# Kernel optimization log

Hardware: AMD Instinct MI355X
Metric: run time of the kernel (lower is better)

The kernel has to match this reference:

```python
import jax, jax.numpy as jnp
import numpy as np

B, L, D, HD, DC = 2, 2048, 2048, 64, 2048
NH = D // HD  # 32 heads


def _rms_norm(x, eps):
    return x * jax.lax.rsqrt(jnp.mean(jnp.square(x), axis=-1, keepdims=True) + eps)


def _apply_rope(x, rope):
    # x: [b,h,l,d]; rope: [2,l,d]. x_hat = interleave(-x_odd, x_even)
    x2 = x.reshape(*x.shape[:-1], HD // 2, 2)
    x_hat = jnp.stack([-x2[..., 1], x2[..., 0]], axis=-1).reshape(x.shape)
    return x * rope[0] + x_hat * rope[1]


def setup_inputs() -> dict:
    key = jax.random.key(0)
    ks = jax.random.split(key, 6)
    return {
        "x": jax.random.normal(ks[0], (B, L, D), jnp.float32),
        "condition": jax.random.normal(ks[1], (B, DC), jnp.float32),
        "rope": jax.random.normal(ks[2], (2, L, HD), jnp.float32),
        "w_ada": jax.random.normal(ks[3], (2 * D, DC), jnp.float32) * 0.02,
        "w_qkv": jax.random.normal(ks[4], (3 * D, D), jnp.float32) * 0.02,
        "w_out": jax.random.normal(ks[5], (D, D), jnp.float32) * 0.02,
        "qk_w": jnp.ones((HD,), jnp.float32),
    }


def reference(x, condition, rope, w_ada, w_qkv, w_out, qk_w):
    eps = jnp.finfo(x.dtype).eps
    # AdaRMSNorm
    ss = (condition @ w_ada.T)[:, None, :]          # [b,1,2D]
    shift, scale = jnp.split(ss, 2, axis=-1)
    h = _rms_norm(x, eps) * (1.0 + scale) + shift   # [b,l,D]
    # fused QKV projection: 'b l (n h d)'
    qkv = (h @ w_qkv.T).reshape(B, L, 3, NH, HD)
    qkv = jnp.transpose(qkv, (2, 0, 3, 1, 4))       # [3,b,h,l,d]
    q, k, v = qkv[0], qkv[1], qkv[2]
    # per-head RMSNorm (with affine weight) + RoPE
    q = _apply_rope(_rms_norm(q, eps) * qk_w, rope)
    k = _apply_rope(_rms_norm(k, eps) * qk_w, rope)
    # SDPA
    scores = jnp.einsum('bhqd,bhkd->bhqk', q, k) / jnp.sqrt(jnp.asarray(HD, x.dtype))
    attn = jax.nn.softmax(scores, axis=-1)
    o = jnp.einsum('bhqk,bhkd->bhqd', attn, v)      # [b,h,l,d]
    o = jnp.transpose(o, (0, 2, 1, 3)).reshape(B, L, D)
    return o @ w_out.T
```

## Files before the change

kernel.cpp:

```cpp
#include <hip/hip_runtime.h>


typedef __bf16 bf16x8 __attribute__((ext_vector_type(8)));
typedef float  f32x4  __attribute__((ext_vector_type(4)));
typedef float  f32x16 __attribute__((ext_vector_type(16)));

#define EPS_F32 1.1920929e-07f
#define QSCALE 0.18033688011112042f

#if defined(__has_builtin)
#  if __has_builtin(__builtin_amdgcn_exp2f)
#    define EXP2F(x) __builtin_amdgcn_exp2f(x)
#  else
#    define EXP2F(x) __expf((x) * 0.6931471805599453f)
#  endif
#  if __has_builtin(__builtin_amdgcn_rcpf)
#    define RCPF(x) __builtin_amdgcn_rcpf(x)
#  else
#    define RCPF(x) (1.0f / (x))
#  endif
#else
#  define EXP2F(x) __expf((x) * 0.6931471805599453f)
#  define RCPF(x) (1.0f / (x))
#endif

__device__ __forceinline__ float bf2f(unsigned int u16) {
  union { unsigned int i; float f; } v; v.i = (u16 & 0xffffu) << 16; return v.f;
}
__device__ __forceinline__ unsigned short f2bf(float f) {
  union { float f; unsigned int i; } v; v.f = f;
  unsigned int r = v.i + 0x7fffu + ((v.i >> 16) & 1u);
  return (unsigned short)(r >> 16);
}
__device__ __forceinline__ unsigned int f2bf_rn_u(float f) {
  union { float f; unsigned int i; } v; v.f = f;
  return v.i + 0x8000u;
}

__device__ __forceinline__ void gload16(const void* g, void* l) {
  __builtin_amdgcn_global_load_lds(
      (const __attribute__((address_space(1))) unsigned int*)(unsigned long long)g,
      (__attribute__((address_space(3))) unsigned int*)(unsigned int)(unsigned long long)l,
      16, 0, 0);
}

__global__ __launch_bounds__(256) void ada_gemm_kernel(
    const float* __restrict__ cond, const float* __restrict__ w_ada,
    float* __restrict__ ss)
{
  const int lane = threadIdx.x & 63;
  const int gw = blockIdx.x * 4 + (threadIdx.x >> 6);
  const int b = gw >> 12;
  const int j = gw & 4095;
  const float4* wr = (const float4*)(w_ada + j * 2048);
  const float4* cr = (const float4*)(cond + b * 2048);
  float acc = 0.f;
  #pragma unroll
  for (int k4 = 0; k4 < 8; ++k4) {
    float4 w = wr[lane + k4 * 64];
    float4 c = cr[lane + k4 * 64];
    acc += w.x * c.x + w.y * c.y + w.z * c.z + w.w * c.w;
  }
  #pragma unroll
  for (int off = 1; off < 64; off <<= 1) acc += __shfl_xor(acc, off);
  if (lane == 0) ss[b * 4096 + j] = acc;
}

__global__ __launch_bounds__(256) void ada_rms_kernel(
    const float* __restrict__ x, const float* __restrict__ ss,
    unsigned short* __restrict__ H)
{
  const int row = blockIdx.x;
  const int b = row >> 11;
  const int tid = threadIdx.x;
  const int lane = tid & 63, wave = tid >> 6;
  const float* xr = x + (size_t)row * 2048;
  float4 v0 = ((const float4*)xr)[tid * 2];
  float4 v1 = ((const float4*)xr)[tid * 2 + 1];
  float ssq = v0.x*v0.x + v0.y*v0.y + v0.z*v0.z + v0.w*v0.w
            + v1.x*v1.x + v1.y*v1.y + v1.z*v1.z + v1.w*v1.w;
  #pragma unroll
  for (int off = 1; off < 64; off <<= 1) ssq += __shfl_xor(ssq, off);
  __shared__ float red[4];
  if (lane == 0) red[wave] = ssq;
  __syncthreads();
  const float tot = red[0] + red[1] + red[2] + red[3];
  const float r = rsqrtf(tot * (1.f / 2048.f) + EPS_F32);
  const int c0 = tid * 8;
  const float* sh = ss + b * 4096;
  float xv[8] = {v0.x, v0.y, v0.z, v0.w, v1.x, v1.y, v1.z, v1.w};
  unsigned int pk[4];
  #pragma unroll
  for (int p = 0; p < 4; ++p) {
    const int c = c0 + p * 2;
    float h0 = xv[p*2+0] * r * (1.f + sh[2048 + c])     + sh[c];
    float h1 = xv[p*2+1] * r * (1.f + sh[2048 + c + 1]) + sh[c + 1];
    pk[p] = (unsigned int)f2bf(h0) | ((unsigned int)f2bf(h1) << 16);
  }
  *(uint4*)&H[(size_t)row * 2048 + c0] = make_uint4(pk[0], pk[1], pk[2], pk[3]);
}

__global__ __launch_bounds__(256) void cast2_kernel(
    const float* __restrict__ a,
    const float* __restrict__ b,
    unsigned short* __restrict__ dst)
{
  const int i = blockIdx.x * 256 + threadIdx.x;
  float4 v = (i < 3145728) ? ((const float4*)a)[i]
                           : ((const float4*)b)[i - 3145728];
  unsigned int p0 = (unsigned int)f2bf(v.x) | ((unsigned int)f2bf(v.y) << 16);
  unsigned int p1 = (unsigned int)f2bf(v.z) | ((unsigned int)f2bf(v.w) << 16);
  *(uint2*)&dst[(size_t)i * 4] = make_uint2(p0, p1);
}

template <int MODE>
__global__ __launch_bounds__(256) void gemm_bt_kernel(
    const unsigned short* __restrict__ A,
    const unsigned short* __restrict__ Bw,
    void* __restrict__ Cv,
    unsigned short* __restrict__ vt,
    int M, int N, int K)
{
  __shared__ unsigned short As[128 * 32];
  __shared__ unsigned short Bs[128 * 32];
  const int tid  = threadIdx.x;
  const int lane = tid & 63;
  const int wave = tid >> 6;
  const int wm = (wave >> 1) * 64;
  const int wn = (wave & 1) * 64;
  const int bm = blockIdx.y * 128;
  const int bn = blockIdx.x * 128;

  f32x4 acc[4][4] = {};

  const int sm = tid >> 2;
  const int sk = (tid & 3) * 8;
  const unsigned short* Ap  = A  + (size_t)(bm + sm) * K + sk;
  const unsigned short* Ap2 = Ap + (size_t)64 * K;
  const unsigned short* Bp  = Bw + (size_t)(bn + sm) * K + sk;
  const unsigned short* Bp2 = Bp + (size_t)64 * K;
  unsigned short* lA  = &As[tid * 8];
  unsigned short* lA2 = &As[tid * 8 + 2048];
  unsigned short* lB  = &Bs[tid * 8];
  unsigned short* lB2 = &Bs[tid * 8 + 2048];

  const int fr = lane & 15;
  const int fk = (lane >> 4) * 8;

  for (int k0 = 0; k0 < K; k0 += 32) {
    __syncthreads();
    gload16(Ap  + k0, lA);
    gload16(Ap2 + k0, lA2);
    gload16(Bp  + k0, lB);
    gload16(Bp2 + k0, lB2);
    __syncthreads();

    bf16x8 af[4], bfr[4];
    #pragma unroll
    for (int i = 0; i < 4; ++i)
      af[i] = *(const bf16x8*)&As[(wm + i * 16 + fr) * 32 + fk];
    #pragma unroll
    for (int j = 0; j < 4; ++j)
      bfr[j] = *(const bf16x8*)&Bs[(wn + j * 16 + fr) * 32 + fk];
    #pragma unroll
    for (int i = 0; i < 4; ++i)
      #pragma unroll
      for (int j = 0; j < 4; ++j)
        acc[i][j] = __builtin_amdgcn_mfma_f32_16x16x32_bf16(af[i], bfr[j], acc[i][j], 0, 0, 0);
  }

  const int cr = (lane >> 4) * 4;
  const int cc = lane & 15;
  if (MODE == 2 && bn >= 4096) {
    #pragma unroll
    for (int i = 0; i < 4; ++i)
      #pragma unroll
      for (int j = 0; j < 4; ++j)
        #pragma unroll
        for (int r = 0; r < 4; ++r) {
          const int m  = bm + wm + i * 16 + cr + r;
          const int dg = bn + wn + j * 16 + cc - 4096;
          const int l  = m & 2047;
          const size_t dst = ((size_t)((m >> 11) * 32 + (dg >> 6)) * 64 + (dg & 63)) * 2048
                           + (l >> 6) * 64 + (l & 15) * 4 + ((l >> 4) & 3);
          vt[dst] = f2bf(acc[i][j][r]);
        }
  } else {
    #pragma unroll
    for (int i = 0; i < 4; ++i)
      #pragma unroll
      for (int j = 0; j < 4; ++j)
        #pragma unroll
        for (int r = 0; r < 4; ++r) {
          const int row = bm + wm + i * 16 + cr + r;
          const int col = bn + wn + j * 16 + cc;
          if (MODE != 0)
            ((unsigned short*)Cv)[(size_t)row * N + col] = f2bf(acc[i][j][r]);
          else
            ((float*)Cv)[(size_t)row * N + col] = acc[i][j][r];
        }
  }
}

__global__ __launch_bounds__(256) void qk_rope_kernel(
    unsigned short* __restrict__ QKV, const float* __restrict__ rope,
    const float* __restrict__ qk_w)
{
  const int lane = threadIdx.x & 63;
  const int gid = blockIdx.x * 4 + (threadIdx.x >> 6);
  const int l = gid & 2047;
  const int h = (gid >> 11) & 31;
  const int b = gid >> 16;
  const int base = (b * 2048 + l) * 6144 + h * 64 + lane;
  const float r0 = rope[l * 64 + lane];
  const float r1 = rope[131072 + l * 64 + lane];
  const float w  = qk_w[lane];
  #pragma unroll
  for (int t = 0; t < 2; ++t) {
    const int idx = base + 2048 * t;
    const float v = bf2f(QKV[idx]);
    float sq = v * v;
    #pragma unroll
    for (int off = 1; off < 64; off <<= 1) sq += __shfl_xor(sq, off);
    const float vn = v * rsqrtf(sq * (1.f / 64.f) + EPS_F32) * w;
    const float vp = __shfl_xor(vn, 1);
    const float vh = (lane & 1) ? vp : -vp;
    const float scale = (t == 0) ? QSCALE : 1.0f;
    QKV[idx] = f2bf((vn * r0 + vh * r1) * scale);
  }
}

__global__ __launch_bounds__(256, 2) void attn_mfma_kernel(
    const unsigned short* __restrict__ QKV,
    const unsigned short* __restrict__ Vt,
    unsigned short* __restrict__ O)
{
  __shared__ unsigned short Ks[64 * 72];
  __shared__ unsigned short Vs[64 * 72];
  __shared__ unsigned short Ps[4 * 64 * 68];
  const int tid  = threadIdx.x;
  const int lane = tid & 63;
  const int wave = tid >> 6;
  const int blk = blockIdx.x;
  const int bh = blk & 63;
  const int qt = blk >> 6;
  const int b = bh >> 5, h = bh & 31;
  const int rowbase = b << 11;
  const int qbase = qt * 256 + wave * 64;

  const int m16  = lane & 15;
  const int quad = lane >> 4;
  const int m32  = lane & 31;
  const int hl   = lane >> 5;

  bf16x8 qf[4][2];
  #pragma unroll
  for (int qi = 0; qi < 4; ++qi)
    #pragma unroll
    for (int ch = 0; ch < 2; ++ch)
      qf[qi][ch] = *(const bf16x8*)&QKV[(size_t)(rowbase + qbase + qi * 16 + m16) * 6144
                                        + h * 64 + ch * 32 + quad * 8];

  const int sr = tid >> 2;
  const int sc = (tid & 3) * 16;
  const unsigned short* Kg = QKV + (size_t)(rowbase + sr) * 6144 + 2048 + h * 64 + sc;
  const unsigned short* Vg = Vt + (size_t)(bh * 64 + sr) * 2048 + sc;

  f32x16 accO[2][2] = {};
  float part[4][4] = {};
  unsigned short* Pw = &Ps[(wave * 64) * 68];

  for (int kt = 0; kt < 32; ++kt) {
    __syncthreads();
    {
      const uint4* kp = (const uint4*)(Kg + (size_t)kt * 64 * 6144);
      const uint4* vp = (const uint4*)(Vg + kt * 64);
      uint4 k0 = kp[0], k1 = kp[1];
      uint4 v0 = vp[0], v1 = vp[1];
      *(uint4*)&Ks[sr * 72 + sc]     = k0;
      *(uint4*)&Ks[sr * 72 + sc + 8] = k1;
      *(uint4*)&Vs[sr * 72 + sc]     = v0;
      *(uint4*)&Vs[sr * 72 + sc + 8] = v1;
    }
    __syncthreads();

    unsigned int pk[4][4][2];
    #pragma unroll
    for (int kj = 0; kj < 4; ++kj) {
      bf16x8 kf0 = *(const bf16x8*)&Ks[(kj * 16 + m16) * 72 + quad * 8];
      bf16x8 kf1 = *(const bf16x8*)&Ks[(kj * 16 + m16) * 72 + 32 + quad * 8];
      #pragma unroll
      for (int qi = 0; qi < 4; ++qi) {
        f32x4 acc = {};
        acc = __builtin_amdgcn_mfma_f32_16x16x32_bf16(qf[qi][0], kf0, acc, 0, 0, 0);
        acc = __builtin_amdgcn_mfma_f32_16x16x32_bf16(qf[qi][1], kf1, acc, 0, 0, 0);
        #pragma unroll
        for (int r = 0; r < 4; ++r) {
          float p = EXP2F(acc[r]);
          part[qi][r] += p;
          unsigned int pb = f2bf_rn_u(p);
          if (kj == 0)      pk[qi][r][0]  = pb >> 16;
          else if (kj == 1) pk[qi][r][0] |= pb & 0xffff0000u;
          else if (kj == 2) pk[qi][r][1]  = pb >> 16;
          else              pk[qi][r][1] |= pb & 0xffff0000u;
        }
      }
    }
    #pragma unroll
    for (int qi = 0; qi < 4; ++qi)
      #pragma unroll
      for (int r = 0; r < 4; ++r)
        *(uint2*)&Pw[(qi * 16 + quad * 4 + r) * 68 + m16 * 4] =
            make_uint2(pk[qi][r][0], pk[qi][r][1]);

    #pragma unroll
    for (int ch = 0; ch < 4; ++ch) {
      bf16x8 pa0 = *(const bf16x8*)&Pw[m32 * 68 + ch * 16 + hl * 8];
      bf16x8 pa1 = *(const bf16x8*)&Pw[(32 + m32) * 68 + ch * 16 + hl * 8];
      bf16x8 vb0 = *(const bf16x8*)&Vs[m32 * 72 + ch * 16 + hl * 8];
      bf16x8 vb1 = *(const bf16x8*)&Vs[(32 + m32) * 72 + ch * 16 + hl * 8];
      accO[0][0] = __builtin_amdgcn_mfma_f32_32x32x16_bf16(pa0, vb0, accO[0][0], 0, 0, 0);
      accO[0][1] = __builtin_amdgcn_mfma_f32_32x32x16_bf16(pa0, vb1, accO[0][1], 0, 0, 0);
      accO[1][0] = __builtin_amdgcn_mfma_f32_32x32x16_bf16(pa1, vb0, accO[1][0], 0, 0, 0);
      accO[1][1] = __builtin_amdgcn_mfma_f32_32x32x16_bf16(pa1, vb1, accO[1][1], 0, 0, 0);
    }
  }

  #pragma unroll
  for (int qi = 0; qi < 4; ++qi)
    #pragma unroll
    for (int r = 0; r < 4; ++r)
      #pragma unroll
      for (int off = 1; off < 16; off <<= 1)
        part[qi][r] += __shfl_xor(part[qi][r], off);

  #pragma unroll
  for (int qs = 0; qs < 2; ++qs) {
    #pragma unroll
    for (int reg = 0; reg < 16; ++reg) {
      const int r = reg & 3;
      const int s = reg >> 2;
      const int qsrc = ((2 * s + hl) & 3) * 16 + m16;
      const float rs = __shfl(part[qs * 2 + (reg >> 3)][r], qsrc);
      const float inv = RCPF(rs);
      const int rho = r + 8 * s + 4 * hl;
      const size_t base = (size_t)(rowbase + qbase + qs * 32 + rho) * 2048 + h * 64;
      O[base + m32]      = f2bf(accO[qs][0][reg] * inv);
      O[base + 32 + m32] = f2bf(accO[qs][1][reg] * inv);
    }
  }
}

extern "C" void kernel_launch(void* const* d_in, const int* in_sizes, int n_in,
                              void* d_out, int out_size, void* d_ws, size_t ws_size,
                              hipStream_t stream) {
  (void)in_sizes; (void)n_in; (void)out_size; (void)ws_size;
  const float* x     = (const float*)d_in[0];
  const float* cond  = (const float*)d_in[1];
  const float* rope  = (const float*)d_in[2];
  const float* w_ada = (const float*)d_in[3];
  const float* w_qkv = (const float*)d_in[4];
  const float* w_out = (const float*)d_in[5];
  const float* qk_w  = (const float*)d_in[6];
  float* out = (float*)d_out;

  char* ws = (char*)d_ws;
  float*          ss   = (float*)ws;
  unsigned short* H    = (unsigned short*)(ws + 32768);
  unsigned short* Wq   = H + 8388608;
  unsigned short* Wo   = Wq + 12582912;
  unsigned short* QKV  = Wo + 4194304;
  unsigned short* Vt_g = QKV + 25165824;

  ada_gemm_kernel<<<2048, 256, 0, stream>>>(cond, w_ada, ss);
  ada_rms_kernel<<<4096, 256, 0, stream>>>(x, ss, H);
  cast2_kernel<<<16384, 256, 0, stream>>>(w_qkv, w_out, Wq);
  gemm_bt_kernel<2><<<dim3(48, 32), 256, 0, stream>>>(H, Wq, (void*)QKV, Vt_g, 4096, 6144, 2048);
  qk_rope_kernel<<<32768, 256, 0, stream>>>(QKV, rope, qk_w);
  attn_mfma_kernel<<<512, 256, 0, stream>>>(QKV, Vt_g, H);
  gemm_bt_kernel<0><<<dim3(16, 32), 256, 0, stream>>>(H, Wo, (void*)out, nullptr, 4096, 2048, 2048);
}
```

Before: 478.0 us.

## Add 256x256-tile 8-wave pipelined QKV GEMM kernel with swizzled LDS

Replaces the generic QKV projection GEMM with a dedicated kernel. It uses 256x256 output tiles, 8 waves per block, double-buffered and XOR-swizzled LDS staging via direct global-to-LDS loads, and an interleaved phase schedule with s_setprio around the MFMA bursts. A block-index swizzle is added for L2 locality. The larger tiles raise data reuse and overlap loads with compute, at the cost of heavy LDS (64KB) and register pressure and hardcoded problem sizes.

```diff
diff --git a/kernel.cpp b/kernel.cpp
--- a/kernel.cpp
+++ b/kernel.cpp
@@ -198,6 +198,148 @@
             ((unsigned short*)Cv)[(size_t)row * N + col] = f2bf(acc[i][j][r]);
           else
             ((float*)Cv)[(size_t)row * N + col] = acc[i][j][r];
+        }
+  }
+}
+
+__global__ __launch_bounds__(512, 2) void gemm_qkv_8p(
+    const unsigned short* __restrict__ A,
+    const unsigned short* __restrict__ Bw,
+    unsigned short* __restrict__ C,
+    unsigned short* __restrict__ vt)
+{
+  __shared__ unsigned short As[2][2][8192];
+  __shared__ unsigned short Bs[2][2][8192];
+
+  const int tid  = threadIdx.x;
+  const int lane = tid & 63;
+  const int wave = tid >> 6;
+  const int wrow = (wave >> 2) * 128;
+  const int wcol = (wave & 3) * 64;
+
+  const int swz = (blockIdx.x & 7) * 48 + (blockIdx.x >> 3);
+  const int bx = swz >> 4;
+  const int by = swz & 15;
+  const int bm = by * 256;
+  const int bn = bx * 256;
+
+  const int fr = lane & 15;
+  const int q_ = lane >> 4;
+  const int laneoff = fr * 32 + ((q_ ^ ((fr >> 1) & 3)) << 3);
+
+  const int rA  = wave * 32 + (lane >> 2);
+  const int kk  = (lane & 3) ^ ((lane >> 3) & 3);
+  const unsigned short* Ag0 = A  + (size_t)(bm + rA) * 2048 + kk * 8;
+  const unsigned short* Ag1 = Ag0 + (size_t)16 * 2048;
+  const unsigned short* Bg0 = Bw + (size_t)(bn + rA) * 2048 + kk * 8;
+  const unsigned short* Bg1 = Bg0 + (size_t)16 * 2048;
+  const int ldso = rA * 32 + (lane & 3) * 8;
+
+  f32x4 acc[8][4] = {};
+  bf16x8 fA[4], fB[4];
+
+#define STAGE_A(SB, SKH, KT) do { \
+    gload16(Ag0 + (KT) * 64 + (SKH) * 32, &As[SB][SKH][ldso]); \
+    gload16(Ag1 + (KT) * 64 + (SKH) * 32, &As[SB][SKH][ldso + 512]); } while (0)
+#define STAGE_B(SB, SKH, KT) do { \
+    gload16(Bg0 + (KT) * 64 + (SKH) * 32, &Bs[SB][SKH][ldso]); \
+    gload16(Bg1 + (KT) * 64 + (SKH) * 32, &Bs[SB][SKH][ldso + 512]); } while (0)
+#define VMW(N) asm volatile("s_waitcnt vmcnt(" #N ")" ::: "memory")
+#define LDB(BUF, KH) do { const unsigned short* p_ = &Bs[BUF][KH][wcol * 32 + laneoff]; \
+    fB[0] = *(const bf16x8*)&p_[0];    fB[1] = *(const bf16x8*)&p_[512]; \
+    fB[2] = *(const bf16x8*)&p_[1024]; fB[3] = *(const bf16x8*)&p_[1536]; } while (0)
+#define LDA(BUF, KH, MH) do { const unsigned short* p_ = &As[BUF][KH][(wrow + (MH) * 64) * 32 + laneoff]; \
+    fA[0] = *(const bf16x8*)&p_[0];    fA[1] = *(const bf16x8*)&p_[512]; \
+    fA[2] = *(const bf16x8*)&p_[1024]; fA[3] = *(const bf16x8*)&p_[1536]; } while (0)
+#define MFMA16(MH) do { \
+    _Pragma("unroll") \
+    for (int f_ = 0; f_ < 4; ++f_) { \
+      _Pragma("unroll") \
+      for (int n_ = 0; n_ < 4; ++n_) \
+        acc[(MH) * 4 + f_][n_] = __builtin_amdgcn_mfma_f32_16x16x32_bf16( \
+            fA[f_], fB[n_], acc[(MH) * 4 + f_][n_], 0, 0, 0); \
+    } } while (0)
+#define PH_MID() do { __builtin_amdgcn_s_barrier(); \
+    asm volatile("s_waitcnt lgkmcnt(0)"); \
+    __builtin_amdgcn_s_setprio(1); } while (0)
+#define PH_END() do { __builtin_amdgcn_s_setprio(0); \
+    __builtin_amdgcn_s_barrier(); } while (0)
+
+  STAGE_A(0, 0, 0); STAGE_B(0, 0, 0); STAGE_A(0, 1, 0); STAGE_B(0, 1, 0);
+  VMW(4);
+  __builtin_amdgcn_s_barrier();
+
+  for (int it = 0; it < 16; ++it) {
+    const int t1 = 2 * it + 1;
+    const int t2 = 2 * it + 2;
+    const bool pf = (it < 15);
+
+    LDB(0, 0); LDA(0, 0, 0);
+    STAGE_A(1, 0, t1);
+    PH_MID(); MFMA16(0); PH_END();
+    LDA(0, 0, 1);
+    STAGE_B(1, 0, t1);
+    VMW(4);
+    PH_MID(); MFMA16(1); PH_END();
+    LDB(0, 1); LDA(0, 1, 0);
+    STAGE_A(1, 1, t1);
+    PH_MID(); MFMA16(0); PH_END();
+    LDA(0, 1, 1);
+    STAGE_B(1, 1, t1);
+    VMW(4);
+    PH_MID(); MFMA16(1); PH_END();
+
+    LDB(1, 0); LDA(1, 0, 0);
+    if (pf) STAGE_A(0, 0, t2);
+    PH_MID(); MFMA16(0); PH_END();
+    LDA(1, 0, 1);
+    if (pf) { STAGE_B(0, 0, t2); VMW(4); }
+    else    { VMW(0); }
+    PH_MID(); MFMA16(1); PH_END();
+    LDB(1, 1); LDA(1, 1, 0);
+    if (pf) STAGE_A(0, 1, t2);
+    PH_MID(); MFMA16(0); PH_END();
+    LDA(1, 1, 1);
+    if (pf) STAGE_B(0, 1, t2);
+    VMW(4);
+    PH_MID(); MFMA16(1); PH_END();
+  }
+
+#undef STAGE_A
+#undef STAGE_B
+#undef VMW
+#undef LDB
+#undef LDA
+#undef MFMA16
+#undef PH_MID
+#undef PH_END
+
+  const int cr = (lane >> 4) * 4;
+  const int cc = lane & 15;
+  if (bn >= 4096) {
+    #pragma unroll
+    for (int mf = 0; mf < 8; ++mf)
+      #pragma unroll
+      for (int nf = 0; nf < 4; ++nf)
+        #pragma unroll
+        for (int r = 0; r < 4; ++r) {
+          const int m  = bm + wrow + mf * 16 + cr + r;
+          const int dg = bn + wcol + nf * 16 + cc - 4096;
+          const int l  = m & 2047;
+          const size_t dst = ((size_t)((m >> 11) * 32 + (dg >> 6)) * 64 + (dg & 63)) * 2048
+                           + (l >> 6) * 64 + (l & 15) * 4 + ((l >> 4) & 3);
+          vt[dst] = f2bf(acc[mf][nf][r]);
+        }
+  } else {
+    #pragma unroll
+    for (int mf = 0; mf < 8; ++mf)
+      #pragma unroll
+      for (int nf = 0; nf < 4; ++nf)
+        #pragma unroll
+        for (int r = 0; r < 4; ++r) {
+          const int row = bm + wrow + mf * 16 + cr + r;
+          const int col = bn + wcol + nf * 16 + cc;
+          C[(size_t)row * 6144 + col] = f2bf(acc[mf][nf][r]);
         }
   }
 }
@@ -375,7 +517,7 @@
   ada_gemm_kernel<<<2048, 256, 0, stream>>>(cond, w_ada, ss);
   ada_rms_kernel<<<4096, 256, 0, stream>>>(x, ss, H);
   cast2_kernel<<<16384, 256, 0, stream>>>(w_qkv, w_out, Wq);
-  gemm_bt_kernel<2><<<dim3(48, 32), 256, 0, stream>>>(H, Wq, (void*)QKV, Vt_g, 4096, 6144, 2048);
+  gemm_qkv_8p<<<384, 512, 0, stream>>>(H, Wq, QKV, Vt_g);
   qk_rope_kernel<<<32768, 256, 0, stream>>>(QKV, rope, qk_w);
   attn_mfma_kernel<<<512, 256, 0, stream>>>(QKV, Vt_g, H);
   gemm_bt_kernel<0><<<dim3(16, 32), 256, 0, stream>>>(H, Wo, (void*)out, nullptr, 4096, 2048, 2048);
```

Result: faster. 467.0 us (-2.3%).
